# Kernel optimization log

Measured on AMD Instinct MI355X. Metric: run time of the kernel, lower is better.

## Reference

```python
import jax, jax.numpy as jnp
import numpy as np

K = 3          # kernel_size
PAD = 1        # padding
FOCAL = 50.0
DMIN = 1.0
DMAX = 50.0
ORIG_H = 512.0  # original_image_size[1]


def setup_inputs() -> dict:
    key = jax.random.key(0)
    k1, k2 = jax.random.split(key)
    x = jax.random.normal(k1, (4, 64, 256, 256), dtype=jnp.float32)
    # conv weight [out_ch, in_ch, K, K] (bias=False)
    W = jax.random.normal(k2, (64, 64, K, K), dtype=jnp.float32) * 0.05
    return {"x": x, "W": W}


def _bilinear(img, xs, ys):
    """Bilinear sample img [B,C,H,W] at float pixel coords xs, ys [B,Ho,Wo].
    Zero padding outside the image (grid_sample semantics)."""
    B, C, H, Wd = img.shape
    Ho, Wo = xs.shape[1], xs.shape[2]
    x0 = jnp.floor(xs); y0 = jnp.floor(ys)
    wx1 = xs - x0; wx0 = 1.0 - wx1
    wy1 = ys - y0; wy0 = 1.0 - wy1
    img_flat = img.reshape(B, C, H * Wd)

    def gat(ix, iy):
        ixi = ix.astype(jnp.int32); iyi = iy.astype(jnp.int32)
        valid = (ixi >= 0) & (ixi < Wd) & (iyi >= 0) & (iyi < H)
        idx = jnp.clip(iyi, 0, H - 1) * Wd + jnp.clip(ixi, 0, Wd - 1)
        v = jnp.take_along_axis(img_flat, idx.reshape(B, 1, Ho * Wo), axis=2)
        v = v.reshape(B, C, Ho, Wo)
        return v * valid[:, None].astype(img.dtype)

    return (gat(x0, y0) * (wx0 * wy0)[:, None]
            + gat(x0 + 1, y0) * (wx1 * wy0)[:, None]
            + gat(x0, y0 + 1) * (wx0 * wy1)[:, None]
            + gat(x0 + 1, y0 + 1) * (wx1 * wy1)[:, None])


def reference(x, W):
    B, C, H, Wd = x.shape
    downsample = ORIG_H / H  # 2.0 for H=256

    # upper branch: plain 3x3 conv, padding 1, no bias
    x_upper = jax.lax.conv_general_dilated(x, W, (1, 1), [(PAD, PAD), (PAD, PAD)])

    # geometry -> clamped depth (geometry_method='max', formulation='depth')
    depth = jnp.clip(jnp.max(x, axis=1), DMIN, DMAX)  # [B,H,W]

    # Frontal homography: Hom01 = I with [1,2] = focal/(downsample*depth);
    # its inverse Hom10 shifts y by -s.
    s = FOCAL / (downsample * depth)  # [B,H,W]

    xi = jnp.arange(Wd, dtype=x.dtype)[None, None, :]
    yi = jnp.arange(H, dtype=x.dtype)[None, :, None]
    xs = jnp.broadcast_to(xi, (B, H, Wd))
    ys = yi - s  # Hom10 applied to pixel coords

    # warp input with per-pixel Hom10 (pass_warped_images=True)
    x2 = _bilinear(x, xs, ys)

    # deformable conv: per-pixel offset from Hom10 is (dx,dy)=(0,-s) for all 9 taps
    x_lower = jnp.zeros_like(x_upper)
    for ky in range(K):
        for kx in range(K):
            sx = xs + (kx - PAD)
            sy = ys + (ky - PAD)
            tap = _bilinear(x2, sx, sy)  # [B,C,H,W]
            x_lower = x_lower + jnp.einsum('bchw,oc->bohw', tap, W[:, :, ky, kx])

    # project with 'min' over the stacked (upper, lower) branches
    return jnp.minimum(x_upper, x_lower)
```

## Files before the change

kernel.cpp:

```cpp
#include <hip/hip_runtime.h>
#include <cmath>

constexpr int BB = 4, CC = 64, HH = 256, WW = 256;
constexpr int WP = 258;
constexpr int C2R = 257;

typedef short short8 __attribute__((ext_vector_type(8)));
typedef float f32x4 __attribute__((ext_vector_type(4)));
#define MFMA_BF16 __builtin_amdgcn_mfma_f32_16x16x32_bf16

union U16x8 { uint4 v; unsigned short h[8]; };
union U16x4 { uint2 v; unsigned short h[4]; };

__device__ inline unsigned short f2bf(float f) {
  unsigned u = __builtin_bit_cast(unsigned, f);
  u += 0x7fffu + ((u >> 16) & 1u);
  return (unsigned short)(u >> 16);
}
__device__ inline unsigned short f2bf_trunc(float f) {
  return (unsigned short)(__builtin_bit_cast(unsigned, f) >> 16);
}
__device__ inline float bf2f(unsigned short h) {
  unsigned u = ((unsigned)h) << 16;
  return __builtin_bit_cast(float, u);
}

__global__ __launch_bounds__(256, 4) void k_pack(const float* __restrict__ x,
                                                 float* __restrict__ s,
                                                 unsigned short* __restrict__ xn) {
  __shared__ float tile[CC * 129];
  __shared__ float pmax[2][128];
  const int t = threadIdx.x;
  const int half = blockIdx.x & 1, y = blockIdx.x >> 1, b = blockIdx.y;
  const int px0 = half * 128;
  const int pxl = t & 127, chb = (t >> 7) * 32;

  const float* base = x + (size_t)b * CC * HH * WW + (size_t)y * WW + px0 + pxl;
  float m = -1e30f;
#pragma unroll 8
  for (int i = 0; i < 32; ++i) {
    float v = base[(size_t)(chb + i) * HH * WW];
    tile[(chb + i) * 129 + pxl] = v;
    m = fmaxf(m, v);
  }
  pmax[t >> 7][pxl] = m;

  uint4* xn4 = (uint4*)xn;
  if (t < 8) {
    int col = half ? (WP - 1) : 0;
    xn4[(((size_t)(b * HH + y) * WP + col) * CC + t * 8) >> 3] =
        make_uint4(0, 0, 0, 0);
  }
  __syncthreads();

  if (t < 128) {
    float mm = fmaxf(pmax[0][t], pmax[1][t]);
    s[(b * HH + y) * WW + px0 + t] = 25.0f / fminf(fmaxf(mm, 1.0f), 50.0f);
  }
#pragma unroll
  for (int g = 0; g < 4; ++g) {
    int px = g * 32 + (t >> 3), c8 = t & 7;
    U16x8 r;
#pragma unroll
    for (int j = 0; j < 8; ++j) r.h[j] = f2bf(tile[(c8 * 8 + j) * 129 + px]);
    xn4[(((size_t)(b * HH + y) * WP + px0 + px + 1) * CC + c8 * 8) >> 3] = r.v;
  }
}

__global__ __launch_bounds__(256) void k_wpack(const float* __restrict__ Wt,
                                               unsigned short* __restrict__ Wp) {
  int gid = blockIdx.x * 256 + threadIdx.x;
  int lane = gid & 63, kc = (gid >> 6) & 1, mt = (gid >> 7) & 3, tap = gid >> 9;
  int o = mt * 16 + (lane & 15);
  int kb = kc * 32 + (lane >> 4) * 8;
  int ky = tap / 3, kx = tap % 3;
  U16x8 r;
#pragma unroll
  for (int j = 0; j < 8; ++j)
    r.h[j] = f2bf(Wt[o * 576 + (kb + j) * 9 + ky * 3 + kx]);
  ((uint4*)Wp)[gid] = r.v;
}

__global__ __launch_bounds__(256, 3) void k_lower(const unsigned short* __restrict__ xn,
                                                  const unsigned short* __restrict__ Wp,
                                                  const float* __restrict__ s,
                                                  unsigned short* __restrict__ c2) {
  __shared__ uint4 lds[3168];
  const int t = threadIdx.x;
  const int ctile = blockIdx.x & 3, tr = blockIdx.x >> 2;
  const int b = blockIdx.y;
  const int r0 = tr * 4 - 1;
  const int colBase = ctile * 64;

  const uint4* xn4 = (const uint4*)xn;
  float w0a[13], w1a[13];
  int o0a[13], o1a[13], la[13];
  bool act[13], va[13];
#pragma unroll
  for (int i = 0; i < 13; ++i) {
    int idx = i * 256 + t;
    act[i] = (idx < 3168);
    int rr_ = idx / 528, rem = idx % 528;
    int col_ = rem >> 3, ch_ = rem & 7;
    int xrow = r0 - 1 + rr_;
    va[i] = act[i] && (xrow >= 0) && (xrow < HH);
    la[i] = (rr_ * 66 + col_) * 8 + (ch_ ^ (col_ & 7));
    float sv = 0.0f;
    int pxc = min(max(colBase + col_ - 1, 0), WW - 1);
    if (va[i]) sv = s[(b * HH + xrow) * WW + pxc];
    float ys = (float)xrow - sv;
    float fy = floorf(ys);
    float wfr = ys - fy;
    int i0 = (int)fy;
    w0a[i] = (i0 >= 0) ? 1.0f - wfr : 0.0f;
    w1a[i] = (i0 + 1 >= 0) ? wfr : 0.0f;
    int a0 = max(i0, 0), a1 = max(i0 + 1, 0);
    o0a[i] = ((b * HH + a0) * WP + colBase + col_) * 8 + ch_;
    o1a[i] = ((b * HH + a1) * WP + colBase + col_) * 8 + ch_;
  }
#pragma unroll
  for (int i = 0; i < 13; ++i) {
    if (act[i]) {
      uint4 v = make_uint4(0, 0, 0, 0);
      if (va[i]) {
        U16x8 u0, u1, rr;
        u0.v = xn4[o0a[i]];
        u1.v = xn4[o1a[i]];
#pragma unroll
        for (int k = 0; k < 8; ++k)
          rr.h[k] = f2bf_trunc(w0a[i] * bf2f(u0.h[k]) + w1a[i] * bf2f(u1.h[k]));
        v = rr.v;
      }
      lds[la[i]] = v;
    }
  }

  const int lane = t & 63, w = t >> 6;
  const int ow = w & 1, rg = w >> 1, lr = rg * 2;
  const int quad = lane >> 4, l15 = lane & 15;
  const uint4* wp4 = (const uint4*)Wp;
  __syncthreads();

#pragma unroll 1
  for (int pp = 0; pp < 2; ++pp) {
    f32x4 acc[2][2][2];
#pragma unroll
    for (int pi = 0; pi < 2; ++pi)
#pragma unroll
      for (int rr = 0; rr < 2; ++rr)
#pragma unroll
        for (int ct = 0; ct < 2; ++ct) acc[pi][rr][ct] = {0.f, 0.f, 0.f, 0.f};

#pragma unroll 1
    for (int kc = 0; kc < 2; ++kc) {
      short8 wf[9][2];
#pragma unroll
      for (int tap = 0; tap < 9; ++tap)
#pragma unroll
        for (int ct = 0; ct < 2; ++ct)
          wf[tap][ct] = __builtin_bit_cast(
              short8, wp4[((tap * 4 + (ow * 2 + ct)) * 2 + kc) * 64 + lane]);
#pragma unroll
      for (int pi = 0; pi < 2; ++pi) {
        int pt = pp * 2 + pi;
#pragma unroll
        for (int ir = 0; ir < 4; ++ir) {
          int ldr = lr + ir;
#pragma unroll
          for (int kx = 0; kx < 3; ++kx) {
            int col = pt * 16 + l15 + kx;
            short8 xf = __builtin_bit_cast(
                short8, lds[(ldr * 66 + col) * 8 + ((kc * 4 + quad) ^ (col & 7))]);
            if (ir <= 2) {
#pragma unroll
              for (int ct = 0; ct < 2; ++ct)
                acc[pi][0][ct] = MFMA_BF16(wf[ir * 3 + kx][ct], xf, acc[pi][0][ct], 0, 0, 0);
            }
            if (ir >= 1) {
#pragma unroll
              for (int ct = 0; ct < 2; ++ct)
                acc[pi][1][ct] = MFMA_BF16(wf[(ir - 1) * 3 + kx][ct], xf, acc[pi][1][ct], 0, 0, 0);
            }
          }
        }
      }
    }
#pragma unroll
    for (int pi = 0; pi < 2; ++pi) {
      int px = colBase + (pp * 2 + pi) * 16 + l15;
#pragma unroll
      for (int rr = 0; rr < 2; ++rr) {
        int r = r0 + lr + rr;
        if (r > 255) continue;
#pragma unroll
        for (int ct = 0; ct < 2; ++ct) {
          f32x4 A = acc[pi][rr][ct];
          int ch = (ow * 2 + ct) * 16 + quad * 4;
          unsigned short h0 = f2bf(A[0]), h1 = f2bf(A[1]), h2 = f2bf(A[2]), h3 = f2bf(A[3]);
          uint2 val = make_uint2((unsigned)h0 | ((unsigned)h1 << 16),
                                 (unsigned)h2 | ((unsigned)h3 << 16));
          *(uint2*)(c2 + (((size_t)(b * C2R + (r + 1)) * WW + px) * CC + ch)) = val;
        }
      }
    }
  }
}

__global__ __launch_bounds__(256, 3) void k_final(const unsigned short* __restrict__ xn,
                                                  const unsigned short* __restrict__ Wp,
                                                  const float* __restrict__ s,
                                                  const unsigned short* __restrict__ c2,
                                                  float* __restrict__ out) {
  __shared__ uint4 lds[3168];
  const int t = threadIdx.x;
  const int ctile = blockIdx.x & 3, tr = blockIdx.x >> 2;
  const int b = blockIdx.y;
  const int y0 = tr * 4;
  const int colBase = ctile * 64;

  const uint4* src4 = (const uint4*)xn;
#pragma unroll
  for (int i = 0; i < 13; ++i) {
    int idx = i * 256 + t;
    if (idx < 3168) {
      int rr_ = idx / 528, rem = idx % 528;
      int col_ = rem >> 3, ch_ = rem & 7;
      int xrow = y0 - 1 + rr_;
      uint4 v = make_uint4(0, 0, 0, 0);
      if (xrow >= 0 && xrow < HH)
        v = src4[((size_t)(b * HH + xrow) * WP + colBase + col_) * 8 + ch_];
      lds[(rr_ * 66 + col_) * 8 + (ch_ ^ (col_ & 7))] = v;
    }
  }

  const int lane = t & 63, w = t >> 6;
  const int ow = w & 1, rg = w >> 1, lr = rg * 2;
  const int quad = lane >> 4, l15 = lane & 15;
  const uint4* wp4 = (const uint4*)Wp;
  __syncthreads();

#pragma unroll 1
  for (int pp = 0; pp < 2; ++pp) {
    f32x4 acc[2][2][2];
#pragma unroll
    for (int pi = 0; pi < 2; ++pi)
#pragma unroll
      for (int rr = 0; rr < 2; ++rr)
#pragma unroll
        for (int ct = 0; ct < 2; ++ct) acc[pi][rr][ct] = {0.f, 0.f, 0.f, 0.f};

#pragma unroll 1
    for (int kc = 0; kc < 2; ++kc) {
      short8 wf[9][2];
#pragma unroll
      for (int tap = 0; tap < 9; ++tap)
#pragma unroll
        for (int ct = 0; ct < 2; ++ct)
          wf[tap][ct] = __builtin_bit_cast(
              short8, wp4[((tap * 4 + (ow * 2 + ct)) * 2 + kc) * 64 + lane]);
#pragma unroll
      for (int pi = 0; pi < 2; ++pi) {
        int pt = pp * 2 + pi;
#pragma unroll
        for (int ir = 0; ir < 4; ++ir) {
          int ldr = lr + ir;
#pragma unroll
          for (int kx = 0; kx < 3; ++kx) {
            int col = pt * 16 + l15 + kx;
            short8 xf = __builtin_bit_cast(
                short8, lds[(ldr * 66 + col) * 8 + ((kc * 4 + quad) ^ (col & 7))]);
            if (ir <= 2) {
#pragma unroll
              for (int ct = 0; ct < 2; ++ct)
                acc[pi][0][ct] = MFMA_BF16(wf[ir * 3 + kx][ct], xf, acc[pi][0][ct], 0, 0, 0);
            }
            if (ir >= 1) {
#pragma unroll
              for (int ct = 0; ct < 2; ++ct)
                acc[pi][1][ct] = MFMA_BF16(wf[(ir - 1) * 3 + kx][ct], xf, acc[pi][1][ct], 0, 0, 0);
            }
          }
        }
      }
    }
#pragma unroll
    for (int pi = 0; pi < 2; ++pi) {
      int px = colBase + (pp * 2 + pi) * 16 + l15;
#pragma unroll
      for (int rr = 0; rr < 2; ++rr) {
        int y = y0 + lr + rr;
        float sv = s[(b * HH + y) * WW + px];
        float ys = (float)y - sv;
        float fy = floorf(ys);
        float wfr = ys - fy;
        int i0 = (int)fy;
        float lw0 = (i0 + 1 >= 0 && i0 + 1 <= HH) ? 1.0f - wfr : 0.0f;
        float lw1 = (i0 + 2 >= 0 && i0 + 2 <= HH) ? wfr : 0.0f;
        int a0 = min(max(i0 + 1, 0), HH);
        int a1 = min(max(i0 + 2, 0), HH);
#pragma unroll
        for (int ct = 0; ct < 2; ++ct) {
          f32x4 A = acc[pi][rr][ct];
          int ch = (ow * 2 + ct) * 16 + quad * 4;
          U16x4 v0, v1;
          v0.v = *(const uint2*)(c2 + ((size_t)(b * C2R + a0) * WW + px) * CC + ch);
          v1.v = *(const uint2*)(c2 + ((size_t)(b * C2R + a1) * WW + px) * CC + ch);
#pragma unroll
          for (int reg = 0; reg < 4; ++reg) {
            float lower = lw0 * bf2f(v0.h[reg]) + lw1 * bf2f(v1.h[reg]);
            out[((size_t)(b * CC + ch + reg) * HH + y) * WW + px] =
                fminf(A[reg], lower);
          }
        }
      }
    }
  }
}

extern "C" void kernel_launch(void* const* d_in, const int* in_sizes, int n_in,
                              void* d_out, int out_size, void* d_ws, size_t ws_size,
                              hipStream_t stream) {
  const float* x = (const float*)d_in[0];
  const float* Wt = (const float*)d_in[1];
  float* out = (float*)d_out;

  char* ws = (char*)d_ws;
  float* s = (float*)ws;
  unsigned short* Wp = (unsigned short*)(ws + 1048576);
  unsigned short* xn = (unsigned short*)(ws + 1122304);
  unsigned short* c2 = (unsigned short*)(ws + 34938880);
  k_pack<<<dim3(HH * 2, BB), 256, 0, stream>>>(x, s, xn);
  k_wpack<<<dim3(18), 256, 0, stream>>>(Wt, Wp);
  k_lower<<<dim3(4 * 65, BB), 256, 0, stream>>>(xn, Wp, s, c2);
  k_final<<<dim3(4 * 64, BB), 256, 0, stream>>>(xn, Wp, s, c2, out);
}
```

Measured before the change: 195.4 us.

## Halve row tile per block, remap waves to column halves, relayout c2

Each block now covers 2 output rows instead of 4, so the grid doubles, LDS per block drops, and occupancy is raised to 4 blocks per CU. Waves now split the 64-column tile into two 32-column halves instead of splitting rows, which removes the outer pp loop. The intermediate c2 buffer changes to a channel-group-major layout ([b][og][row][px] of 4-channel uint2), so stores and gathers walk contiguous pixels. The cost is more halo rows recomputed and reloaded per output row (4 LDS rows for 2 outputs instead of 6 for 4), and more blocks to launch.

```diff
diff --git a/kernel.cpp b/kernel.cpp
--- a/kernel.cpp
+++ b/kernel.cpp
@@ -81,148 +81,148 @@
   ((uint4*)Wp)[gid] = r.v;
 }
 
-__global__ __launch_bounds__(256, 3) void k_lower(const unsigned short* __restrict__ xn,
+__global__ __launch_bounds__(256, 4) void k_lower(const unsigned short* __restrict__ xn,
                                                   const unsigned short* __restrict__ Wp,
                                                   const float* __restrict__ s,
                                                   unsigned short* __restrict__ c2) {
-  __shared__ uint4 lds[3168];
+  __shared__ uint4 lds[2112];
   const int t = threadIdx.x;
   const int ctile = blockIdx.x & 3, tr = blockIdx.x >> 2;
   const int b = blockIdx.y;
-  const int r0 = tr * 4 - 1;
+  const int r0 = tr * 2 - 1;
   const int colBase = ctile * 64;
 
   const uint4* xn4 = (const uint4*)xn;
-  float w0a[13], w1a[13];
-  int o0a[13], o1a[13], la[13];
-  bool act[13], va[13];
-#pragma unroll
-  for (int i = 0; i < 13; ++i) {
-    int idx = i * 256 + t;
-    act[i] = (idx < 3168);
-    int rr_ = idx / 528, rem = idx % 528;
-    int col_ = rem >> 3, ch_ = rem & 7;
-    int xrow = r0 - 1 + rr_;
-    va[i] = act[i] && (xrow >= 0) && (xrow < HH);
-    la[i] = (rr_ * 66 + col_) * 8 + (ch_ ^ (col_ & 7));
-    float sv = 0.0f;
-    int pxc = min(max(colBase + col_ - 1, 0), WW - 1);
-    if (va[i]) sv = s[(b * HH + xrow) * WW + pxc];
-    float ys = (float)xrow - sv;
-    float fy = floorf(ys);
-    float wfr = ys - fy;
-    int i0 = (int)fy;
-    w0a[i] = (i0 >= 0) ? 1.0f - wfr : 0.0f;
-    w1a[i] = (i0 + 1 >= 0) ? wfr : 0.0f;
-    int a0 = max(i0, 0), a1 = max(i0 + 1, 0);
-    o0a[i] = ((b * HH + a0) * WP + colBase + col_) * 8 + ch_;
-    o1a[i] = ((b * HH + a1) * WP + colBase + col_) * 8 + ch_;
-  }
-#pragma unroll
-  for (int i = 0; i < 13; ++i) {
-    if (act[i]) {
-      uint4 v = make_uint4(0, 0, 0, 0);
-      if (va[i]) {
-        U16x8 u0, u1, rr;
-        u0.v = xn4[o0a[i]];
-        u1.v = xn4[o1a[i]];
-#pragma unroll
-        for (int k = 0; k < 8; ++k)
-          rr.h[k] = f2bf_trunc(w0a[i] * bf2f(u0.h[k]) + w1a[i] * bf2f(u1.h[k]));
-        v = rr.v;
-      }
-      lds[la[i]] = v;
+#pragma unroll 1
+  for (int g = 0; g < 3; ++g) {
+    float w0a[3], w1a[3];
+    int o0a[3], o1a[3], la[3];
+    bool act[3], va[3];
+#pragma unroll
+    for (int j = 0; j < 3; ++j) {
+      int idx = (g * 3 + j) * 256 + t;
+      act[j] = idx < 2112;
+      int rr_ = idx / 528, rem = idx % 528;
+      int col_ = rem >> 3, ch_ = rem & 7;
+      int xrow = r0 - 1 + rr_;
+      va[j] = act[j] && (xrow >= 0) && (xrow < HH);
+      la[j] = (rr_ * 66 + col_) * 8 + (ch_ ^ (col_ & 7));
+      float sv = 0.0f;
+      int pxc = min(max(colBase + col_ - 1, 0), WW - 1);
+      if (va[j]) sv = s[(b * HH + min(max(xrow, 0), HH - 1)) * WW + pxc];
+      float ys = (float)xrow - sv;
+      float fy = floorf(ys);
+      float wfr = ys - fy;
+      int i0 = (int)fy;
+      w0a[j] = (i0 >= 0) ? 1.0f - wfr : 0.0f;
+      w1a[j] = (i0 + 1 >= 0) ? wfr : 0.0f;
+      int a0 = min(max(i0, 0), HH - 1), a1 = min(max(i0 + 1, 0), HH - 1);
+      o0a[j] = ((b * HH + a0) * WP + colBase + col_) * 8 + ch_;
+      o1a[j] = ((b * HH + a1) * WP + colBase + col_) * 8 + ch_;
+    }
+#pragma unroll
+    for (int j = 0; j < 3; ++j) {
+      if (act[j]) {
+        uint4 v = make_uint4(0, 0, 0, 0);
+        if (va[j]) {
+          U16x8 u0, u1, rr;
+          u0.v = xn4[o0a[j]];
+          u1.v = xn4[o1a[j]];
+#pragma unroll
+          for (int k = 0; k < 8; ++k)
+            rr.h[k] = f2bf_trunc(w0a[j] * bf2f(u0.h[k]) + w1a[j] * bf2f(u1.h[k]));
+          v = rr.v;
+        }
+        lds[la[j]] = v;
+      }
     }
   }
 
   const int lane = t & 63, w = t >> 6;
-  const int ow = w & 1, rg = w >> 1, lr = rg * 2;
+  const int ow = w & 1, ch2 = w >> 1;
   const int quad = lane >> 4, l15 = lane & 15;
   const uint4* wp4 = (const uint4*)Wp;
   __syncthreads();
 
+  f32x4 acc[2][2][2];
+#pragma unroll
+  for (int pt = 0; pt < 2; ++pt)
+#pragma unroll
+    for (int rr = 0; rr < 2; ++rr)
+#pragma unroll
+      for (int ct = 0; ct < 2; ++ct) acc[pt][rr][ct] = {0.f, 0.f, 0.f, 0.f};
+
 #pragma unroll 1
-  for (int pp = 0; pp < 2; ++pp) {
-    f32x4 acc[2][2][2];
-#pragma unroll
-    for (int pi = 0; pi < 2; ++pi)
-#pragma unroll
-      for (int rr = 0; rr < 2; ++rr)
-#pragma unroll
-        for (int ct = 0; ct < 2; ++ct) acc[pi][rr][ct] = {0.f, 0.f, 0.f, 0.f};
-
-#pragma unroll 1
-    for (int kc = 0; kc < 2; ++kc) {
-      short8 wf[9][2];
-#pragma unroll
-      for (int tap = 0; tap < 9; ++tap)
-#pragma unroll
-        for (int ct = 0; ct < 2; ++ct)
-          wf[tap][ct] = __builtin_bit_cast(
-              short8, wp4[((tap * 4 + (ow * 2 + ct)) * 2 + kc) * 64 + lane]);
-#pragma unroll
-      for (int pi = 0; pi < 2; ++pi) {
-        int pt = pp * 2 + pi;
-#pragma unroll
-        for (int ir = 0; ir < 4; ++ir) {
-          int ldr = lr + ir;
-#pragma unroll
-          for (int kx = 0; kx < 3; ++kx) {
-            int col = pt * 16 + l15 + kx;
-            short8 xf = __builtin_bit_cast(
-                short8, lds[(ldr * 66 + col) * 8 + ((kc * 4 + quad) ^ (col & 7))]);
-            if (ir <= 2) {
-#pragma unroll
-              for (int ct = 0; ct < 2; ++ct)
-                acc[pi][0][ct] = MFMA_BF16(wf[ir * 3 + kx][ct], xf, acc[pi][0][ct], 0, 0, 0);
-            }
-            if (ir >= 1) {
-#pragma unroll
-              for (int ct = 0; ct < 2; ++ct)
-                acc[pi][1][ct] = MFMA_BF16(wf[(ir - 1) * 3 + kx][ct], xf, acc[pi][1][ct], 0, 0, 0);
-            }
+  for (int kc = 0; kc < 2; ++kc) {
+    short8 wf[9][2];
+#pragma unroll
+    for (int tap = 0; tap < 9; ++tap)
+#pragma unroll
+      for (int ct = 0; ct < 2; ++ct)
+        wf[tap][ct] = __builtin_bit_cast(
+            short8, wp4[((tap * 4 + (ow * 2 + ct)) * 2 + kc) * 64 + lane]);
+#pragma unroll
+    for (int pt = 0; pt < 2; ++pt) {
+#pragma unroll
+      for (int ir = 0; ir < 4; ++ir) {
+#pragma unroll
+        for (int kx = 0; kx < 3; ++kx) {
+          int col = ch2 * 32 + pt * 16 + l15 + kx;
+          short8 xf = __builtin_bit_cast(
+              short8, lds[(ir * 66 + col) * 8 + ((kc * 4 + quad) ^ (col & 7))]);
+          if (ir <= 2) {
+#pragma unroll
+            for (int ct = 0; ct < 2; ++ct)
+              acc[pt][0][ct] = MFMA_BF16(wf[ir * 3 + kx][ct], xf, acc[pt][0][ct], 0, 0, 0);
+          }
+          if (ir >= 1) {
+#pragma unroll
+            for (int ct = 0; ct < 2; ++ct)
+              acc[pt][1][ct] = MFMA_BF16(wf[(ir - 1) * 3 + kx][ct], xf, acc[pt][1][ct], 0, 0, 0);
           }
         }
       }
     }
-#pragma unroll
-    for (int pi = 0; pi < 2; ++pi) {
-      int px = colBase + (pp * 2 + pi) * 16 + l15;
-#pragma unroll
-      for (int rr = 0; rr < 2; ++rr) {
-        int r = r0 + lr + rr;
-        if (r > 255) continue;
-#pragma unroll
-        for (int ct = 0; ct < 2; ++ct) {
-          f32x4 A = acc[pi][rr][ct];
-          int ch = (ow * 2 + ct) * 16 + quad * 4;
-          unsigned short h0 = f2bf(A[0]), h1 = f2bf(A[1]), h2 = f2bf(A[2]), h3 = f2bf(A[3]);
-          uint2 val = make_uint2((unsigned)h0 | ((unsigned)h1 << 16),
-                                 (unsigned)h2 | ((unsigned)h3 << 16));
-          *(uint2*)(c2 + (((size_t)(b * C2R + (r + 1)) * WW + px) * CC + ch)) = val;
-        }
-      }
-    }
-  }
-}
-
-__global__ __launch_bounds__(256, 3) void k_final(const unsigned short* __restrict__ xn,
+  }
+
+  uint2* c2u = (uint2*)c2;
+#pragma unroll
+  for (int pt = 0; pt < 2; ++pt) {
+    int px = colBase + ch2 * 32 + pt * 16 + l15;
+#pragma unroll
+    for (int rr = 0; rr < 2; ++rr) {
+      int r = r0 + rr;
+      if (r > 255) continue;
+#pragma unroll
+      for (int ct = 0; ct < 2; ++ct) {
+        f32x4 A = acc[pt][rr][ct];
+        int og = (ow * 2 + ct) * 4 + quad;
+        unsigned short h0 = f2bf(A[0]), h1 = f2bf(A[1]), h2 = f2bf(A[2]), h3 = f2bf(A[3]);
+        uint2 val = make_uint2((unsigned)h0 | ((unsigned)h1 << 16),
+                               (unsigned)h2 | ((unsigned)h3 << 16));
+        c2u[(size_t)((b * 16 + og) * C2R + (r + 1)) * WW + px] = val;
+      }
+    }
+  }
+}
+
+__global__ __launch_bounds__(256, 4) void k_final(const unsigned short* __restrict__ xn,
                                                   const unsigned short* __restrict__ Wp,
                                                   const float* __restrict__ s,
                                                   const unsigned short* __restrict__ c2,
                                                   float* __restrict__ out) {
-  __shared__ uint4 lds[3168];
+  __shared__ uint4 lds[2112];
   const int t = threadIdx.x;
   const int ctile = blockIdx.x & 3, tr = blockIdx.x >> 2;
   const int b = blockIdx.y;
-  const int y0 = tr * 4;
+  const int y0 = tr * 2;
   const int colBase = ctile * 64;
 
   const uint4* src4 = (const uint4*)xn;
-#pragma unroll
-  for (int i = 0; i < 13; ++i) {
+#pragma unroll 1
+  for (int i = 0; i < 9; ++i) {
     int idx = i * 256 + t;
-    if (idx < 3168) {
+    if (idx < 2112) {
       int rr_ = idx / 528, rem = idx % 528;
       int col_ = rem >> 3, ch_ = rem & 7;
       int xrow = y0 - 1 + rr_;
@@ -234,83 +234,80 @@
   }
 
   const int lane = t & 63, w = t >> 6;
-  const int ow = w & 1, rg = w >> 1, lr = rg * 2;
+  const int ow = w & 1, ch2 = w >> 1;
   const int quad = lane >> 4, l15 = lane & 15;
   const uint4* wp4 = (const uint4*)Wp;
   __syncthreads();
 
+  f32x4 acc[2][2][2];
+#pragma unroll
+  for (int pt = 0; pt < 2; ++pt)
+#pragma unroll
+    for (int rr = 0; rr < 2; ++rr)
+#pragma unroll
+      for (int ct = 0; ct < 2; ++ct) acc[pt][rr][ct] = {0.f, 0.f, 0.f, 0.f};
+
 #pragma unroll 1
-  for (int pp = 0; pp < 2; ++pp) {
-    f32x4 acc[2][2][2];
-#pragma unroll
-    for (int pi = 0; pi < 2; ++pi)
-#pragma unroll
-      for (int rr = 0; rr < 2; ++rr)
-#pragma unroll
-        for (int ct = 0; ct < 2; ++ct) acc[pi][rr][ct] = {0.f, 0.f, 0.f, 0.f};
-
-#pragma unroll 1
-    for (int kc = 0; kc < 2; ++kc) {
-      short8 wf[9][2];
-#pragma unroll
-      for (int tap = 0; tap < 9; ++tap)
-#pragma unroll
-        for (int ct = 0; ct < 2; ++ct)
-          wf[tap][ct] = __builtin_bit_cast(
-              short8, wp4[((tap * 4 + (ow * 2 + ct)) * 2 + kc) * 64 + lane]);
-#pragma unroll
-      for (int pi = 0; pi < 2; ++pi) {
-        int pt = pp * 2 + pi;
-#pragma unroll
-        for (int ir = 0; ir < 4; ++ir) {
-          int ldr = lr + ir;
-#pragma unroll
-          for (int kx = 0; kx < 3; ++kx) {
-            int col = pt * 16 + l15 + kx;
-            short8 xf = __builtin_bit_cast(
-                short8, lds[(ldr * 66 + col) * 8 + ((kc * 4 + quad) ^ (col & 7))]);
-            if (ir <= 2) {
-#pragma unroll
-              for (int ct = 0; ct < 2; ++ct)
-                acc[pi][0][ct] = MFMA_BF16(wf[ir * 3 + kx][ct], xf, acc[pi][0][ct], 0, 0, 0);
-            }
-            if (ir >= 1) {
-#pragma unroll
-              for (int ct = 0; ct < 2; ++ct)
-                acc[pi][1][ct] = MFMA_BF16(wf[(ir - 1) * 3 + kx][ct], xf, acc[pi][1][ct], 0, 0, 0);
-            }
+  for (int kc = 0; kc < 2; ++kc) {
+    short8 wf[9][2];
+#pragma unroll
+    for (int tap = 0; tap < 9; ++tap)
+#pragma unroll
+      for (int ct = 0; ct < 2; ++ct)
+        wf[tap][ct] = __builtin_bit_cast(
+            short8, wp4[((tap * 4 + (ow * 2 + ct)) * 2 + kc) * 64 + lane]);
+#pragma unroll
+    for (int pt = 0; pt < 2; ++pt) {
+#pragma unroll
+      for (int ir = 0; ir < 4; ++ir) {
+#pragma unroll
+        for (int kx = 0; kx < 3; ++kx) {
+          int col = ch2 * 32 + pt * 16 + l15 + kx;
+          short8 xf = __builtin_bit_cast(
+              short8, lds[(ir * 66 + col) * 8 + ((kc * 4 + quad) ^ (col & 7))]);
+          if (ir <= 2) {
+#pragma unroll
+            for (int ct = 0; ct < 2; ++ct)
+              acc[pt][0][ct] = MFMA_BF16(wf[ir * 3 + kx][ct], xf, acc[pt][0][ct], 0, 0, 0);
+          }
+          if (ir >= 1) {
+#pragma unroll
+            for (int ct = 0; ct < 2; ++ct)
+              acc[pt][1][ct] = MFMA_BF16(wf[(ir - 1) * 3 + kx][ct], xf, acc[pt][1][ct], 0, 0, 0);
           }
         }
       }
     }
-#pragma unroll
-    for (int pi = 0; pi < 2; ++pi) {
-      int px = colBase + (pp * 2 + pi) * 16 + l15;
-#pragma unroll
-      for (int rr = 0; rr < 2; ++rr) {
-        int y = y0 + lr + rr;
-        float sv = s[(b * HH + y) * WW + px];
-        float ys = (float)y - sv;
-        float fy = floorf(ys);
-        float wfr = ys - fy;
-        int i0 = (int)fy;
-        float lw0 = (i0 + 1 >= 0 && i0 + 1 <= HH) ? 1.0f - wfr : 0.0f;
-        float lw1 = (i0 + 2 >= 0 && i0 + 2 <= HH) ? wfr : 0.0f;
-        int a0 = min(max(i0 + 1, 0), HH);
-        int a1 = min(max(i0 + 2, 0), HH);
-#pragma unroll
-        for (int ct = 0; ct < 2; ++ct) {
-          f32x4 A = acc[pi][rr][ct];
-          int ch = (ow * 2 + ct) * 16 + quad * 4;
-          U16x4 v0, v1;
-          v0.v = *(const uint2*)(c2 + ((size_t)(b * C2R + a0) * WW + px) * CC + ch);
-          v1.v = *(const uint2*)(c2 + ((size_t)(b * C2R + a1) * WW + px) * CC + ch);
-#pragma unroll
-          for (int reg = 0; reg < 4; ++reg) {
-            float lower = lw0 * bf2f(v0.h[reg]) + lw1 * bf2f(v1.h[reg]);
-            out[((size_t)(b * CC + ch + reg) * HH + y) * WW + px] =
-                fminf(A[reg], lower);
-          }
+  }
+
+  const uint2* c2u = (const uint2*)c2;
+#pragma unroll
+  for (int pt = 0; pt < 2; ++pt) {
+    int px = colBase + ch2 * 32 + pt * 16 + l15;
+#pragma unroll
+    for (int rr = 0; rr < 2; ++rr) {
+      int y = y0 + rr;
+      float sv = s[(b * HH + y) * WW + px];
+      float ys = (float)y - sv;
+      float fy = floorf(ys);
+      float wfr = ys - fy;
+      int i0 = (int)fy;
+      float lw0 = (i0 + 1 >= 0 && i0 + 1 <= HH) ? 1.0f - wfr : 0.0f;
+      float lw1 = (i0 + 2 >= 0 && i0 + 2 <= HH) ? wfr : 0.0f;
+      int a0 = min(max(i0 + 1, 0), HH);
+      int a1 = min(max(i0 + 2, 0), HH);
+#pragma unroll
+      for (int ct = 0; ct < 2; ++ct) {
+        f32x4 A = acc[pt][rr][ct];
+        int og = (ow * 2 + ct) * 4 + quad;
+        U16x4 v0, v1;
+        v0.v = c2u[(size_t)((b * 16 + og) * C2R + a0) * WW + px];
+        v1.v = c2u[(size_t)((b * 16 + og) * C2R + a1) * WW + px];
+#pragma unroll
+        for (int reg = 0; reg < 4; ++reg) {
+          float lower = lw0 * bf2f(v0.h[reg]) + lw1 * bf2f(v1.h[reg]);
+          out[((size_t)(b * CC + og * 4 + reg) * HH + y) * WW + px] =
+              fminf(A[reg], lower);
         }
       }
     }
@@ -331,6 +328,6 @@
   unsigned short* c2 = (unsigned short*)(ws + 34938880);
   k_pack<<<dim3(HH * 2, BB), 256, 0, stream>>>(x, s, xn);
   k_wpack<<<dim3(18), 256, 0, stream>>>(Wt, Wp);
-  k_lower<<<dim3(4 * 65, BB), 256, 0, stream>>>(xn, Wp, s, c2);
-  k_final<<<dim3(4 * 64, BB), 256, 0, stream>>>(xn, Wp, s, c2, out);
-}
+  k_lower<<<dim3(4 * 129, BB), 256, 0, stream>>>(xn, Wp, s, c2);
+  k_final<<<dim3(4 * 128, BB), 256, 0, stream>>>(xn, Wp, s, c2, out);
+}
```

Result: faster. 190.2 us (-2.7%).
